# Performance work log

Hardware: AMD Instinct MI355X
Metric: run time of the kernel (lower is better)

## Reference

```python
import jax, jax.numpy as jnp
import numpy as np

N_NODES = 100000
N_EDGES = 1600000


def _degree_norms(src, dst, n):
    ones = jnp.ones(src.shape[0], dtype=jnp.float32)
    deg_out = jax.ops.segment_sum(ones, src, num_segments=n)
    deg_in = jax.ops.segment_sum(ones, dst, num_segments=n)
    src_norm = jax.lax.rsqrt(jnp.maximum(deg_out, 1.0))
    dst_norm = jax.lax.rsqrt(jnp.maximum(deg_in, 1.0))
    return src_norm, dst_norm


def _graph_conv(x, W, b, src, dst, src_norm, dst_norm, n):
    # DGL GraphConv, norm='both': D_dst^{-1/2} A D_src^{-1/2} X W + b
    # Apply W first (same math, smaller messages).
    h = x @ W                                  # [N, out]
    m = (h * src_norm[:, None])[src]           # [E, out] gather
    agg = jax.ops.segment_sum(m, dst, num_segments=n)  # [N, out] scatter-add
    return agg * dst_norm[:, None] + b


def setup_inputs() -> dict:
    key = jax.random.key(0)
    ks = jax.random.split(key, 10)
    inp = {
        "x": jax.random.normal(ks[0], (N_NODES, 128), dtype=jnp.float32),
        "src": jax.random.randint(ks[1], (N_EDGES,), 0, N_NODES, dtype=jnp.int32),
        "dst": jax.random.randint(ks[2], (N_EDGES,), 0, N_NODES, dtype=jnp.int32),
        "W1": jax.random.normal(ks[3], (128, 64), dtype=jnp.float32) * 0.08,
        "b1": jnp.zeros((64,), dtype=jnp.float32),
        "W2": jax.random.normal(ks[4], (64, 64), dtype=jnp.float32) * 0.12,
        "b2": jnp.zeros((64,), dtype=jnp.float32),
        "W3": jax.random.normal(ks[5], (64, 64), dtype=jnp.float32) * 0.12,
        "b3": jnp.zeros((64,), dtype=jnp.float32),
        "W4": jax.random.normal(ks[6], (64, 64), dtype=jnp.float32) * 0.12,
        "b4": jnp.zeros((64,), dtype=jnp.float32),
        "Wres": jax.random.normal(ks[7], (128, 64), dtype=jnp.float32) * 0.08,
        "bres": jnp.zeros((64,), dtype=jnp.float32),
        "Wop": jax.random.normal(ks[8], (64, 16), dtype=jnp.float32) * 0.12,
        "bop": jnp.zeros((16,), dtype=jnp.float32),
    }
    return inp


def reference(x, src, dst, W1, b1, W2, b2, W3, b3, W4, b4, Wres, bres, Wop, bop):
    n = x.shape[0]
    src_norm, dst_norm = _degree_norms(src, dst, n)
    res = x @ Wres + bres
    out = jax.nn.relu(_graph_conv(x, W1, b1, src, dst, src_norm, dst_norm, n))
    out = jax.nn.relu(_graph_conv(out, W2, b2, src, dst, src_norm, dst_norm, n))
    out = jax.nn.relu(_graph_conv(out, W3, b3, src, dst, src_norm, dst_norm, n))
    out = _graph_conv(out, W4, b4, src, dst, src_norm, dst_norm, n)
    out = jax.nn.relu(out + res)
    return out @ Wop + bop
```

## Files before the change

kernel.cpp:

```cpp
#include <hip/hip_runtime.h>
#include <cstdint>
#include <cstddef>


#define SLOTS 64
#define BCAP 5120
#define ACHUNK 4096

typedef __attribute__((ext_vector_type(8))) short bf16x8;
typedef __attribute__((ext_vector_type(4))) float f32x4;

__device__ __forceinline__ unsigned short f2bf(float f) {
  union { float f; unsigned u; } v; v.f = f;
  unsigned r = (v.u + 0x7fffu + ((v.u >> 16) & 1u)) >> 16;
  return (unsigned short)r;
}
__device__ __forceinline__ float bf2f(unsigned short h) {
  union { unsigned u; float f; } v; v.u = ((unsigned)h) << 16;
  return v.f;
}
__device__ __forceinline__ void bf2x2(unsigned u, float* lo, float* hi) {
  union { unsigned x; float f; } a, b;
  a.x = u << 16; b.x = u & 0xFFFF0000u;
  *lo = a.f; *hi = b.f;
}

__global__ void prep_kernel(const float* __restrict__ W1, const float* __restrict__ W2,
                            const float* __restrict__ W3, const float* __restrict__ W4,
                            const float* __restrict__ Wres,
                            unsigned short* __restrict__ WT,
                            int* __restrict__ gcur_d, int* __restrict__ gcur_s, int nbuck) {
  int i = blockIdx.x * blockDim.x + threadIdx.x;
  if (i < nbuck) { gcur_d[i] = 0; gcur_s[i] = 0; }
  if (i < 8192) {
    int c = i >> 7, k = i & 127;
    WT[i] = f2bf(W1[k * 64 + c]);
  } else if (i < 12288) {
    int j = i - 8192; int c = j >> 6, k = j & 63;
    WT[i] = f2bf(W2[k * 64 + c]);
  } else if (i < 16384) {
    int j = i - 12288; int c = j >> 6, k = j & 63;
    WT[i] = f2bf(W3[k * 64 + c]);
  } else if (i < 20480) {
    int j = i - 16384; int c = j >> 6, k = j & 63;
    WT[i] = f2bf(W4[k * 64 + c]);
  } else if (i < 28672) {
    int j = i - 20480; int c = j >> 7, k = j & 127;
    WT[i] = f2bf(Wres[k * 64 + c]);
  }
}

__global__ __launch_bounds__(256) void bucket_kernel(
    const int* __restrict__ src, const int* __restrict__ dst,
    int* __restrict__ gcur_d, int* __restrict__ gcur_s,
    unsigned* __restrict__ dbuck, unsigned char* __restrict__ sbuck,
    int E, int nbuck) {
  __shared__ int s_src[ACHUNK];
  __shared__ int s_dst[ACHUNK];
  __shared__ int run_d[512];
  __shared__ int run_s[512];
  const int t = threadIdx.x;
  const int base = blockIdx.x * ACHUNK;
  int cnt = E - base;
  if (cnt > ACHUNK) cnt = ACHUNK;

  for (int i = t; i < cnt; i += 256) {
    s_src[i] = src[base + i];
    s_dst[i] = dst[base + i];
  }
  for (int i = t; i < nbuck; i += 256) { run_d[i] = 0; run_s[i] = 0; }
  __syncthreads();
  for (int i = t; i < cnt; i += 256) {
    atomicAdd(&run_d[s_dst[i] >> 8], 1);
    atomicAdd(&run_s[s_src[i] >> 8], 1);
  }
  __syncthreads();
  {
    const int iters = (nbuck + 255) >> 8;
    for (int it = 0; it < iters; ++it) {
      int i = it * 256 + t;
      int hd = 0, hs = 0;
      if (i < nbuck) { hd = run_d[i]; hs = run_s[i]; }
      __syncthreads();
      if (i < nbuck) {
        run_d[i] = hd ? atomicAdd(&gcur_d[i], hd) : 0;
        run_s[i] = hs ? atomicAdd(&gcur_s[i], hs) : 0;
      }
      __syncthreads();
    }
  }
  for (int i = t; i < cnt; i += 256) {
    int d = s_dst[i], s = s_src[i];
    int bd = d >> 8;
    int pd = atomicAdd(&run_d[bd], 1);
    if (pd < BCAP) dbuck[(size_t)bd * BCAP + pd] = ((unsigned)(d & 255) << 24) | (unsigned)s;
    int bs = s >> 8;
    int ps = atomicAdd(&run_s[bs], 1);
    if (ps < BCAP) sbuck[(size_t)bs * BCAP + ps] = (unsigned char)(s & 255);
  }
}

__global__ __launch_bounds__(256) void csr_kernel(
    const unsigned* __restrict__ dbuck, const int* __restrict__ gcur_d,
    int* __restrict__ col, int* __restrict__ cnt_arr,
    float* __restrict__ dnorm, int N) {
  __shared__ int cur[256];
  const int b = blockIdx.x;
  const int t = threadIdx.x;
  const int node0 = b << 8;
  cur[t] = 0;
  __syncthreads();
  int cnt = gcur_d[b];
  if (cnt > BCAP) cnt = BCAP;
  const unsigned* p = dbuck + (size_t)b * BCAP;
  for (int i = t; i < cnt; i += 256) {
    unsigned e = p[i];
    int nl = e >> 24;
    int s = (int)(e & 0x00FFFFFFu);
    int pos = atomicAdd(&cur[nl], 1);
    if (pos < SLOTS) col[(size_t)(node0 + nl) * SLOTS + pos] = s;
  }
  __syncthreads();
  int node = node0 + t;
  if (node < N) {
    int c = cur[t];
    cnt_arr[node] = c;
    float d = (float)(c < 1 ? 1 : c);
    dnorm[node] = rsqrtf(d);
  }
}

__global__ __launch_bounds__(256) void degout_kernel(
    const unsigned char* __restrict__ sbuck, const int* __restrict__ gcur_s,
    float* __restrict__ snorm, int N) {
  __shared__ int cur[256];
  const int b = blockIdx.x;
  const int t = threadIdx.x;
  cur[t] = 0;
  __syncthreads();
  int cnt = gcur_s[b];
  if (cnt > BCAP) cnt = BCAP;
  const unsigned char* p = sbuck + (size_t)b * BCAP;
  for (int i = t; i < cnt; i += 256) atomicAdd(&cur[p[i]], 1);
  __syncthreads();
  int node = (b << 8) + t;
  if (node < N) {
    int c = cur[t];
    snorm[node] = rsqrtf((float)(c < 1 ? 1 : c));
  }
}

__global__ __launch_bounds__(256) void gemm_mfma_kernel(
    const unsigned short* __restrict__ X, const unsigned short* __restrict__ WT,
    const float* __restrict__ norm, unsigned short* __restrict__ out, int n) {
  __shared__ float ol[64][68];
  const int t = threadIdx.x;
  const int l = t & 63;
  const int w = t >> 6;
  const int node0 = blockIdx.x * 64;
  const int row = l & 15, kg = l >> 4;

  int arow = node0 + w * 16 + row;
  if (arow > n - 1) arow = n - 1;
  const unsigned short* ab = X + (size_t)arow * 64 + kg * 8;
  bf16x8 a0 = *(const bf16x8*)(ab);
  bf16x8 a1 = *(const bf16x8*)(ab + 32);

  f32x4 acc[4];
#pragma unroll
  for (int ct = 0; ct < 4; ct++) acc[ct] = (f32x4){0.f, 0.f, 0.f, 0.f};

#pragma unroll
  for (int ct = 0; ct < 4; ct++) {
    const unsigned short* wb = WT + (size_t)(ct * 16 + row) * 64 + kg * 8;
    bf16x8 b0 = *(const bf16x8*)(wb);
    bf16x8 b1 = *(const bf16x8*)(wb + 32);
    acc[ct] = __builtin_amdgcn_mfma_f32_16x16x32_bf16(a0, b0, acc[ct], 0, 0, 0);
    acc[ct] = __builtin_amdgcn_mfma_f32_16x16x32_bf16(a1, b1, acc[ct], 0, 0, 0);
  }

#pragma unroll
  for (int ct = 0; ct < 4; ct++)
#pragma unroll
    for (int i = 0; i < 4; i++)
      ol[w * 16 + kg * 4 + i][ct * 16 + row] = acc[ct][i];
  __syncthreads();

  {
    int r2 = t >> 2, cg = (t & 3) * 16;
    int node = node0 + r2;
    if (node < n) {
      float s = norm[node];
      unsigned short o[16];
#pragma unroll
      for (int i = 0; i < 16; i++) o[i] = f2bf(ol[r2][cg + i] * s);
      *(uint4*)&out[(size_t)node * 64 + cg] = *(const uint4*)&o[0];
      *(uint4*)&out[(size_t)node * 64 + cg + 8] = *(const uint4*)&o[8];
    }
  }
}

__global__ __launch_bounds__(256) void gemm1_mfma_kernel(
    const float* __restrict__ X, const unsigned short* __restrict__ W1T,
    const unsigned short* __restrict__ WresT, const float* __restrict__ bres,
    const float* __restrict__ norm,
    unsigned short* __restrict__ Hout, unsigned short* __restrict__ Rout, int n) {
  __shared__ unsigned short in_bf[64][136];
  __shared__ float ol[64][68];
  const int t = threadIdx.x;
  const int l = t & 63;
  const int w = t >> 6;
  const int node0 = blockIdx.x * 64;
  const int row = l & 15, kg = l >> 4;

  {
    int r = t >> 2, cb = (t & 3) * 32;
    int gi = node0 + r;
    unsigned short tmp[32];
    if (gi < n) {
      const float* s = X + (size_t)gi * 128 + cb;
#pragma unroll
      for (int q = 0; q < 32; q += 4) {
        float4 f = *(const float4*)(s + q);
        tmp[q] = f2bf(f.x); tmp[q + 1] = f2bf(f.y);
        tmp[q + 2] = f2bf(f.z); tmp[q + 3] = f2bf(f.w);
      }
    } else {
#pragma unroll
      for (int q = 0; q < 32; q++) tmp[q] = 0;
    }
#pragma unroll
    for (int q = 0; q < 32; q += 8)
      *(uint4*)&in_bf[r][cb + q] = *(const uint4*)&tmp[q];
  }
  __syncthreads();

  bf16x8 a[4];
#pragma unroll
  for (int kh = 0; kh < 4; kh++)
    a[kh] = *(const bf16x8*)&in_bf[w * 16 + row][kh * 32 + kg * 8];

  f32x4 acc[4], acc2[4];
#pragma unroll
  for (int ct = 0; ct < 4; ct++) {
    acc[ct] = (f32x4){0.f, 0.f, 0.f, 0.f};
    acc2[ct] = (f32x4){0.f, 0.f, 0.f, 0.f};
  }

#pragma unroll
  for (int kh = 0; kh < 4; kh++) {
#pragma unroll
    for (int ct = 0; ct < 4; ct++) {
      const unsigned short* wb1 = W1T + (size_t)(ct * 16 + row) * 128 + kh * 32 + kg * 8;
      const unsigned short* wbr = WresT + (size_t)(ct * 16 + row) * 128 + kh * 32 + kg * 8;
      bf16x8 b1 = *(const bf16x8*)(wb1);
      bf16x8 br = *(const bf16x8*)(wbr);
      acc[ct] = __builtin_amdgcn_mfma_f32_16x16x32_bf16(a[kh], b1, acc[ct], 0, 0, 0);
      acc2[ct] = __builtin_amdgcn_mfma_f32_16x16x32_bf16(a[kh], br, acc2[ct], 0, 0, 0);
    }
  }

#pragma unroll
  for (int ct = 0; ct < 4; ct++)
#pragma unroll
    for (int i = 0; i < 4; i++)
      ol[w * 16 + kg * 4 + i][ct * 16 + row] = acc[ct][i];
  __syncthreads();
  {
    int r2 = t >> 2, cg = (t & 3) * 16;
    int node = node0 + r2;
    if (node < n) {
      float s = norm[node];
      unsigned short o[16];
#pragma unroll
      for (int i = 0; i < 16; i++) o[i] = f2bf(ol[r2][cg + i] * s);
      *(uint4*)&Hout[(size_t)node * 64 + cg] = *(const uint4*)&o[0];
      *(uint4*)&Hout[(size_t)node * 64 + cg + 8] = *(const uint4*)&o[8];
    }
  }
  __syncthreads();

#pragma unroll
  for (int ct = 0; ct < 4; ct++)
#pragma unroll
    for (int i = 0; i < 4; i++)
      ol[w * 16 + kg * 4 + i][ct * 16 + row] = acc2[ct][i];
  __syncthreads();
  {
    int r2 = t >> 2, cg = (t & 3) * 16;
    int node = node0 + r2;
    if (node < n) {
      unsigned short o[16];
#pragma unroll
      for (int i = 0; i < 16; i++) o[i] = f2bf(ol[r2][cg + i] + bres[cg + i]);
      *(uint4*)&Rout[(size_t)node * 64 + cg] = *(const uint4*)&o[0];
      *(uint4*)&Rout[(size_t)node * 64 + cg + 8] = *(const uint4*)&o[8];
    }
  }
}

#define UNPACK_ADD(u, A)                         \
  { float f0, f1, f2, f3;                        \
    bf2x2((u).x, &f0, &f1);                      \
    bf2x2((u).y, &f2, &f3);                      \
    A[0] += f0; A[1] += f1; A[2] += f2; A[3] += f3; }

template <int RELU>
__global__ __launch_bounds__(256) void agg_kernel(
    const unsigned short* __restrict__ H, const int* __restrict__ cnt_arr,
    const int* __restrict__ col, const float* __restrict__ dnorm,
    const float* __restrict__ bias, unsigned short* __restrict__ O,
    int n) {
  const int lane = threadIdx.x & 63;
  const int g = lane >> 4;
  const int fl = lane & 15;
  const int wave = (blockIdx.x * blockDim.x + threadIdx.x) >> 6;
  const int nwaves = (gridDim.x * blockDim.x) >> 6;
  const uint2* __restrict__ H2 = (const uint2*)H;
  const float4 bb = ((const float4*)bias)[fl];

  for (int v0 = wave * 2; v0 < n; v0 += nwaves * 2) {
    const int v1 = v0 + 1;
    int cnt0 = cnt_arr[v0];
    int cnt1 = (v1 < n) ? cnt_arr[v1] : 0;
    if (cnt0 > SLOTS) cnt0 = SLOTS;
    if (cnt1 > SLOTS) cnt1 = SLOTS;
    const int* cp0 = col + (size_t)v0 * SLOTS;
    const int* cp1 = (v1 < n) ? col + (size_t)v1 * SLOTS : cp0;
    float a0[4] = {0.f, 0.f, 0.f, 0.f};
    float b0[4] = {0.f, 0.f, 0.f, 0.f};
    float a1[4] = {0.f, 0.f, 0.f, 0.f};
    float b1[4] = {0.f, 0.f, 0.f, 0.f};
    const int cmax = cnt0 > cnt1 ? cnt0 : cnt1;
    for (int j = 0; j < cmax; j += 16) {
      const int e0 = j + g;
      const int e1 = j + 4 + g;
      const int e2 = j + 8 + g;
      const int e3 = j + 12 + g;
      int c00 = cp0[e0], c01 = cp0[e1], c02 = cp0[e2], c03 = cp0[e3];
      int c10 = cp1[e0], c11 = cp1[e1], c12 = cp1[e2], c13 = cp1[e3];
      if (e0 < cnt0) { uint2 u = H2[(size_t)c00 * 16 + fl]; UNPACK_ADD(u, a0) }
      if (e1 < cnt0) { uint2 u = H2[(size_t)c01 * 16 + fl]; UNPACK_ADD(u, b0) }
      if (e2 < cnt0) { uint2 u = H2[(size_t)c02 * 16 + fl]; UNPACK_ADD(u, a0) }
      if (e3 < cnt0) { uint2 u = H2[(size_t)c03 * 16 + fl]; UNPACK_ADD(u, b0) }
      if (e0 < cnt1) { uint2 u = H2[(size_t)c10 * 16 + fl]; UNPACK_ADD(u, a1) }
      if (e1 < cnt1) { uint2 u = H2[(size_t)c11 * 16 + fl]; UNPACK_ADD(u, b1) }
      if (e2 < cnt1) { uint2 u = H2[(size_t)c12 * 16 + fl]; UNPACK_ADD(u, a1) }
      if (e3 < cnt1) { uint2 u = H2[(size_t)c13 * 16 + fl]; UNPACK_ADD(u, b1) }
    }
    float r0[4], r1[4];
#pragma unroll
    for (int i = 0; i < 4; i++) {
      float s0 = a0[i] + b0[i];
      s0 += __shfl_xor(s0, 16);
      s0 += __shfl_xor(s0, 32);
      r0[i] = s0;
      float s1 = a1[i] + b1[i];
      s1 += __shfl_xor(s1, 16);
      s1 += __shfl_xor(s1, 32);
      r1[i] = s1;
    }
    if (g == 0) {
      float d = dnorm[v0];
      float q0 = r0[0] * d + bb.x;
      float q1 = r0[1] * d + bb.y;
      float q2 = r0[2] * d + bb.z;
      float q3 = r0[3] * d + bb.w;
      if (RELU) {
        q0 = fmaxf(q0, 0.f); q1 = fmaxf(q1, 0.f);
        q2 = fmaxf(q2, 0.f); q3 = fmaxf(q3, 0.f);
      }
      ushort4 o;
      o.x = f2bf(q0); o.y = f2bf(q1); o.z = f2bf(q2); o.w = f2bf(q3);
      *(ushort4*)&O[(size_t)v0 * SLOTS + 4 * fl] = o;
    } else if (g == 1 && v1 < n) {
      float d = dnorm[v1];
      float q0 = r1[0] * d + bb.x;
      float q1 = r1[1] * d + bb.y;
      float q2 = r1[2] * d + bb.z;
      float q3 = r1[3] * d + bb.w;
      if (RELU) {
        q0 = fmaxf(q0, 0.f); q1 = fmaxf(q1, 0.f);
        q2 = fmaxf(q2, 0.f); q3 = fmaxf(q3, 0.f);
      }
      ushort4 o;
      o.x = f2bf(q0); o.y = f2bf(q1); o.z = f2bf(q2); o.w = f2bf(q3);
      *(ushort4*)&O[(size_t)v1 * SLOTS + 4 * fl] = o;
    }
  }
}

__global__ __launch_bounds__(256) void final_kernel(
    const unsigned short* __restrict__ O4, const unsigned short* __restrict__ R,
    const float* __restrict__ Wop, const float* __restrict__ bop,
    float* __restrict__ out, int n) {
  __shared__ float t_lds[64][68];
  __shared__ float wop_lds[64][16];
  const int t = threadIdx.x;
  const int node0 = blockIdx.x * 64;
  const int srow = t >> 2;
  const int scol = (t & 3) * 16;

  ((float4*)&wop_lds[0][0])[t] = ((const float4*)Wop)[t];

  {
    int gi = node0 + srow;
    float f[16];
    if (gi < n) {
      const unsigned short* po = O4 + (size_t)gi * 64 + scol;
      const unsigned short* pr = R + (size_t)gi * 64 + scol;
      uint4 uo0 = *(const uint4*)(po + 0);
      uint4 uo1 = *(const uint4*)(po + 8);
      uint4 ur0 = *(const uint4*)(pr + 0);
      uint4 ur1 = *(const uint4*)(pr + 8);
      float o0, o1, rr0, rr1;
#define ADDRELU2(UO, UR, idx)                         \
      bf2x2(UO, &o0, &o1); bf2x2(UR, &rr0, &rr1);     \
      f[idx] = fmaxf(o0 + rr0, 0.f);                  \
      f[idx + 1] = fmaxf(o1 + rr1, 0.f);
      ADDRELU2(uo0.x, ur0.x, 0)  ADDRELU2(uo0.y, ur0.y, 2)
      ADDRELU2(uo0.z, ur0.z, 4)  ADDRELU2(uo0.w, ur0.w, 6)
      ADDRELU2(uo1.x, ur1.x, 8)  ADDRELU2(uo1.y, ur1.y, 10)
      ADDRELU2(uo1.z, ur1.z, 12) ADDRELU2(uo1.w, ur1.w, 14)
#undef ADDRELU2
    } else {
#pragma unroll
      for (int j = 0; j < 16; j++) f[j] = 0.f;
    }
#pragma unroll
    for (int j = 0; j < 16; j += 4)
      *(float4*)&t_lds[srow][scol + j] = make_float4(f[j], f[j+1], f[j+2], f[j+3]);
  }
  __syncthreads();

  {
    int nn = t >> 2;
    int fg = t & 3;
    float4 a = ((const float4*)bop)[fg];
#pragma unroll 16
    for (int k = 0; k < 64; k++) {
      float tv = t_lds[nn][k];
      float4 w = *(const float4*)&wop_lds[k][fg * 4];
      a.x = fmaf(tv, w.x, a.x);
      a.y = fmaf(tv, w.y, a.y);
      a.z = fmaf(tv, w.z, a.z);
      a.w = fmaf(tv, w.w, a.w);
    }
    int node = node0 + nn;
    if (node < n) *(float4*)&out[(size_t)node * 16 + fg * 4] = a;
  }
}

extern "C" void kernel_launch(void* const* d_in, const int* in_sizes, int n_in,
                              void* d_out, int out_size, void* d_ws, size_t ws_size,
                              hipStream_t stream) {
  const float* x    = (const float*)d_in[0];
  const int*   src  = (const int*)d_in[1];
  const int*   dst  = (const int*)d_in[2];
  const float* W1   = (const float*)d_in[3];
  const float* b1   = (const float*)d_in[4];
  const float* W2   = (const float*)d_in[5];
  const float* b2   = (const float*)d_in[6];
  const float* W3   = (const float*)d_in[7];
  const float* b3   = (const float*)d_in[8];
  const float* W4   = (const float*)d_in[9];
  const float* b4   = (const float*)d_in[10];
  const float* Wres = (const float*)d_in[11];
  const float* bres = (const float*)d_in[12];
  const float* Wop  = (const float*)d_in[13];
  const float* bop  = (const float*)d_in[14];
  float* out = (float*)d_out;

  const int N = in_sizes[0] / 128;
  const int E = in_sizes[1];
  const int nbuck = (N + 255) >> 8;

  char* p = (char*)d_ws;
  auto alloc = [&](size_t b) {
    char* r = p;
    p += (b + 255) & ~(size_t)255;
    return r;
  };
  int*            gcur_d  = (int*)alloc((size_t)nbuck * 4);
  int*            gcur_s  = (int*)alloc((size_t)nbuck * 4);
  unsigned short* WT      = (unsigned short*)alloc(28672 * 2);
  unsigned*       dbuck   = (unsigned*)alloc((size_t)nbuck * BCAP * 4);
  unsigned char*  sbuck   = (unsigned char*)alloc((size_t)nbuck * BCAP);
  int*            col     = (int*)alloc((size_t)N * SLOTS * 4);
  int*            cnt_arr = (int*)alloc((size_t)N * 4);
  float*          snorm   = (float*)alloc((size_t)N * 4);
  float*          dnorm   = (float*)alloc((size_t)N * 4);
  unsigned short* Hbuf    = (unsigned short*)alloc((size_t)N * 64 * 2);
  unsigned short* Obuf    = (unsigned short*)alloc((size_t)N * 64 * 2);
  unsigned short* Rbuf    = (unsigned short*)alloc((size_t)N * 64 * 2);

  unsigned short* W1T   = WT;
  unsigned short* W2T   = WT + 8192;
  unsigned short* W3T   = WT + 12288;
  unsigned short* W4T   = WT + 16384;
  unsigned short* WresT = WT + 20480;

  prep_kernel<<<112, 256, 0, stream>>>(W1, W2, W3, W4, Wres, WT, gcur_d, gcur_s, nbuck);

  int ga = (E + ACHUNK - 1) / ACHUNK;
  bucket_kernel<<<ga, 256, 0, stream>>>(src, dst, gcur_d, gcur_s, dbuck, sbuck, E, nbuck);
  csr_kernel<<<nbuck, 256, 0, stream>>>(dbuck, gcur_d, col, cnt_arr, dnorm, N);
  degout_kernel<<<nbuck, 256, 0, stream>>>(sbuck, gcur_s, snorm, N);

  int gb = (N + 63) / 64;
  gemm1_mfma_kernel<<<gb, 256, 0, stream>>>(x, W1T, WresT, bres, snorm, Hbuf, Rbuf, N);
  agg_kernel<1><<<2048, 256, 0, stream>>>(Hbuf, cnt_arr, col, dnorm, b1, Obuf, N);
  gemm_mfma_kernel<<<gb, 256, 0, stream>>>(Obuf, W2T, snorm, Hbuf, N);
  agg_kernel<1><<<2048, 256, 0, stream>>>(Hbuf, cnt_arr, col, dnorm, b2, Obuf, N);
  gemm_mfma_kernel<<<gb, 256, 0, stream>>>(Obuf, W3T, snorm, Hbuf, N);
  agg_kernel<1><<<2048, 256, 0, stream>>>(Hbuf, cnt_arr, col, dnorm, b3, Obuf, N);
  gemm_mfma_kernel<<<gb, 256, 0, stream>>>(Obuf, W4T, snorm, Hbuf, N);
  agg_kernel<0><<<2048, 256, 0, stream>>>(Hbuf, cnt_arr, col, dnorm, b4, Obuf, N);
  final_kernel<<<gb, 256, 0, stream>>>(Obuf, Rbuf, Wop, bop, out, N);
}
```

Before: 326.7 us.

## Fuse aggregation with next-layer GEMM and final projection, shuffle-broadcast column indices

Each layer's neighbor aggregation now runs in a 512-thread block that covers 64 nodes. The block writes the ReLU'd bf16 result to LDS and immediately applies the next layer's weight with MFMA plus the source norm, so the intermediate Obuf round trip and the separate GEMM launches go away. The last aggregation is fused with the residual add, ReLU and output projection. Column indices are loaded once per wave and broadcast with shuffles instead of repeated global loads. The first GEMM converts fp32 input straight into registers rather than staging it through LDS. The cost is a fixed node-to-block mapping, which loses the grid-stride load balancing and uses less per-wave ILP (8 edges per iteration instead of 16).

```diff
diff --git a/kernel.cpp b/kernel.cpp
--- a/kernel.cpp
+++ b/kernel.cpp
@@ -15,15 +15,25 @@
   unsigned r = (v.u + 0x7fffu + ((v.u >> 16) & 1u)) >> 16;
   return (unsigned short)r;
 }
-__device__ __forceinline__ float bf2f(unsigned short h) {
-  union { unsigned u; float f; } v; v.u = ((unsigned)h) << 16;
-  return v.f;
-}
 __device__ __forceinline__ void bf2x2(unsigned u, float* lo, float* hi) {
   union { unsigned x; float f; } a, b;
   a.x = u << 16; b.x = u & 0xFFFF0000u;
   *lo = a.f; *hi = b.f;
 }
+__device__ __forceinline__ bf16x8 cvt8(float4 f0, float4 f1) {
+  bf16x8 v;
+  v[0] = (short)f2bf(f0.x); v[1] = (short)f2bf(f0.y);
+  v[2] = (short)f2bf(f0.z); v[3] = (short)f2bf(f0.w);
+  v[4] = (short)f2bf(f1.x); v[5] = (short)f2bf(f1.y);
+  v[6] = (short)f2bf(f1.z); v[7] = (short)f2bf(f1.w);
+  return v;
+}
+
+#define UNPACK_ADD(u, A)                         \
+  { float f0_, f1_, f2_, f3_;                    \
+    bf2x2((u).x, &f0_, &f1_);                    \
+    bf2x2((u).y, &f2_, &f3_);                    \
+    A[0] += f0_; A[1] += f1_; A[2] += f2_; A[3] += f3_; }
 
 __global__ void prep_kernel(const float* __restrict__ W1, const float* __restrict__ W2,
                             const float* __restrict__ W3, const float* __restrict__ W4,
@@ -150,9 +160,11 @@
   }
 }
 
-__global__ __launch_bounds__(256) void gemm_mfma_kernel(
-    const unsigned short* __restrict__ X, const unsigned short* __restrict__ WT,
-    const float* __restrict__ norm, unsigned short* __restrict__ out, int n) {
+__global__ __launch_bounds__(256) void gemm1_mfma_kernel(
+    const float* __restrict__ X, const unsigned short* __restrict__ W1T,
+    const unsigned short* __restrict__ WresT, const float* __restrict__ bres,
+    const float* __restrict__ norm,
+    unsigned short* __restrict__ Hout, unsigned short* __restrict__ Rout, int n) {
   __shared__ float ol[64][68];
   const int t = threadIdx.x;
   const int l = t & 63;
@@ -162,83 +174,14 @@
 
   int arow = node0 + w * 16 + row;
   if (arow > n - 1) arow = n - 1;
-  const unsigned short* ab = X + (size_t)arow * 64 + kg * 8;
-  bf16x8 a0 = *(const bf16x8*)(ab);
-  bf16x8 a1 = *(const bf16x8*)(ab + 32);
-
-  f32x4 acc[4];
-#pragma unroll
-  for (int ct = 0; ct < 4; ct++) acc[ct] = (f32x4){0.f, 0.f, 0.f, 0.f};
-
-#pragma unroll
-  for (int ct = 0; ct < 4; ct++) {
-    const unsigned short* wb = WT + (size_t)(ct * 16 + row) * 64 + kg * 8;
-    bf16x8 b0 = *(const bf16x8*)(wb);
-    bf16x8 b1 = *(const bf16x8*)(wb + 32);
-    acc[ct] = __builtin_amdgcn_mfma_f32_16x16x32_bf16(a0, b0, acc[ct], 0, 0, 0);
-    acc[ct] = __builtin_amdgcn_mfma_f32_16x16x32_bf16(a1, b1, acc[ct], 0, 0, 0);
-  }
-
-#pragma unroll
-  for (int ct = 0; ct < 4; ct++)
-#pragma unroll
-    for (int i = 0; i < 4; i++)
-      ol[w * 16 + kg * 4 + i][ct * 16 + row] = acc[ct][i];
-  __syncthreads();
-
-  {
-    int r2 = t >> 2, cg = (t & 3) * 16;
-    int node = node0 + r2;
-    if (node < n) {
-      float s = norm[node];
-      unsigned short o[16];
-#pragma unroll
-      for (int i = 0; i < 16; i++) o[i] = f2bf(ol[r2][cg + i] * s);
-      *(uint4*)&out[(size_t)node * 64 + cg] = *(const uint4*)&o[0];
-      *(uint4*)&out[(size_t)node * 64 + cg + 8] = *(const uint4*)&o[8];
-    }
-  }
-}
-
-__global__ __launch_bounds__(256) void gemm1_mfma_kernel(
-    const float* __restrict__ X, const unsigned short* __restrict__ W1T,
-    const unsigned short* __restrict__ WresT, const float* __restrict__ bres,
-    const float* __restrict__ norm,
-    unsigned short* __restrict__ Hout, unsigned short* __restrict__ Rout, int n) {
-  __shared__ unsigned short in_bf[64][136];
-  __shared__ float ol[64][68];
-  const int t = threadIdx.x;
-  const int l = t & 63;
-  const int w = t >> 6;
-  const int node0 = blockIdx.x * 64;
-  const int row = l & 15, kg = l >> 4;
-
-  {
-    int r = t >> 2, cb = (t & 3) * 32;
-    int gi = node0 + r;
-    unsigned short tmp[32];
-    if (gi < n) {
-      const float* s = X + (size_t)gi * 128 + cb;
-#pragma unroll
-      for (int q = 0; q < 32; q += 4) {
-        float4 f = *(const float4*)(s + q);
-        tmp[q] = f2bf(f.x); tmp[q + 1] = f2bf(f.y);
-        tmp[q + 2] = f2bf(f.z); tmp[q + 3] = f2bf(f.w);
-      }
-    } else {
-#pragma unroll
-      for (int q = 0; q < 32; q++) tmp[q] = 0;
-    }
-#pragma unroll
-    for (int q = 0; q < 32; q += 8)
-      *(uint4*)&in_bf[r][cb + q] = *(const uint4*)&tmp[q];
-  }
-  __syncthreads();
-
+  const float* ap = X + (size_t)arow * 128 + kg * 8;
   bf16x8 a[4];
 #pragma unroll
-  for (int kh = 0; kh < 4; kh++)
-    a[kh] = *(const bf16x8*)&in_bf[w * 16 + row][kh * 32 + kg * 8];
+  for (int kh = 0; kh < 4; kh++) {
+    float4 f0 = *(const float4*)(ap + kh * 32);
+    float4 f1 = *(const float4*)(ap + kh * 32 + 4);
+    a[kh] = cvt8(f0, f1);
+  }
 
   f32x4 acc[4], acc2[4];
 #pragma unroll
@@ -279,7 +222,6 @@
     }
   }
   __syncthreads();
-
 #pragma unroll
   for (int ct = 0; ct < 4; ct++)
 #pragma unroll
@@ -299,54 +241,46 @@
   }
 }
 
-#define UNPACK_ADD(u, A)                         \
-  { float f0, f1, f2, f3;                        \
-    bf2x2((u).x, &f0, &f1);                      \
-    bf2x2((u).y, &f2, &f3);                      \
-    A[0] += f0; A[1] += f1; A[2] += f2; A[3] += f3; }
-
-template <int RELU>
-__global__ __launch_bounds__(256) void agg_kernel(
+__global__ __launch_bounds__(512) void agg_gemm_kernel(
     const unsigned short* __restrict__ H, const int* __restrict__ cnt_arr,
     const int* __restrict__ col, const float* __restrict__ dnorm,
-    const float* __restrict__ bias, unsigned short* __restrict__ O,
-    int n) {
-  const int lane = threadIdx.x & 63;
-  const int g = lane >> 4;
+    const float* __restrict__ bias, const unsigned short* __restrict__ WTn,
+    const float* __restrict__ snorm, unsigned short* __restrict__ Hn, int N) {
+  __shared__ unsigned short ot[64][72];
+  const int t = threadIdx.x;
+  const int w = t >> 6;
+  const int lane = t & 63;
+  const int sub = lane >> 4;
   const int fl = lane & 15;
-  const int wave = (blockIdx.x * blockDim.x + threadIdx.x) >> 6;
-  const int nwaves = (gridDim.x * blockDim.x) >> 6;
+  const int node0 = blockIdx.x * 64;
   const uint2* __restrict__ H2 = (const uint2*)H;
   const float4 bb = ((const float4*)bias)[fl];
 
-  for (int v0 = wave * 2; v0 < n; v0 += nwaves * 2) {
-    const int v1 = v0 + 1;
-    int cnt0 = cnt_arr[v0];
-    int cnt1 = (v1 < n) ? cnt_arr[v1] : 0;
+  for (int p = 0; p < 4; p++) {
+    const int r0i = w * 8 + p * 2;
+    const int v0 = node0 + r0i, v1 = v0 + 1;
+    int cnt0 = (v0 < N) ? cnt_arr[v0] : 0;
+    int cnt1 = (v1 < N) ? cnt_arr[v1] : 0;
     if (cnt0 > SLOTS) cnt0 = SLOTS;
     if (cnt1 > SLOTS) cnt1 = SLOTS;
-    const int* cp0 = col + (size_t)v0 * SLOTS;
-    const int* cp1 = (v1 < n) ? col + (size_t)v1 * SLOTS : cp0;
+    int cv0 = (lane < cnt0) ? col[(size_t)v0 * SLOTS + lane] : 0;
+    int cv1 = (lane < cnt1) ? col[(size_t)v1 * SLOTS + lane] : 0;
     float a0[4] = {0.f, 0.f, 0.f, 0.f};
     float b0[4] = {0.f, 0.f, 0.f, 0.f};
     float a1[4] = {0.f, 0.f, 0.f, 0.f};
     float b1[4] = {0.f, 0.f, 0.f, 0.f};
     const int cmax = cnt0 > cnt1 ? cnt0 : cnt1;
-    for (int j = 0; j < cmax; j += 16) {
-      const int e0 = j + g;
-      const int e1 = j + 4 + g;
-      const int e2 = j + 8 + g;
-      const int e3 = j + 12 + g;
-      int c00 = cp0[e0], c01 = cp0[e1], c02 = cp0[e2], c03 = cp0[e3];
-      int c10 = cp1[e0], c11 = cp1[e1], c12 = cp1[e2], c13 = cp1[e3];
+    for (int j = 0; j < cmax; j += 8) {
+      const int e0 = j + sub;
+      const int e1 = j + 4 + sub;
+      int c00 = __shfl(cv0, e0);
+      int c01 = __shfl(cv0, e1);
+      int c10 = __shfl(cv1, e0);
+      int c11 = __shfl(cv1, e1);
       if (e0 < cnt0) { uint2 u = H2[(size_t)c00 * 16 + fl]; UNPACK_ADD(u, a0) }
+      if (e0 < cnt1) { uint2 u = H2[(size_t)c10 * 16 + fl]; UNPACK_ADD(u, a1) }
       if (e1 < cnt0) { uint2 u = H2[(size_t)c01 * 16 + fl]; UNPACK_ADD(u, b0) }
-      if (e2 < cnt0) { uint2 u = H2[(size_t)c02 * 16 + fl]; UNPACK_ADD(u, a0) }
-      if (e3 < cnt0) { uint2 u = H2[(size_t)c03 * 16 + fl]; UNPACK_ADD(u, b0) }
-      if (e0 < cnt1) { uint2 u = H2[(size_t)c10 * 16 + fl]; UNPACK_ADD(u, a1) }
       if (e1 < cnt1) { uint2 u = H2[(size_t)c11 * 16 + fl]; UNPACK_ADD(u, b1) }
-      if (e2 < cnt1) { uint2 u = H2[(size_t)c12 * 16 + fl]; UNPACK_ADD(u, a1) }
-      if (e3 < cnt1) { uint2 u = H2[(size_t)c13 * 16 + fl]; UNPACK_ADD(u, b1) }
     }
     float r0[4], r1[4];
 #pragma unroll
@@ -360,94 +294,190 @@
       s1 += __shfl_xor(s1, 32);
       r1[i] = s1;
     }
-    if (g == 0) {
-      float d = dnorm[v0];
-      float q0 = r0[0] * d + bb.x;
-      float q1 = r0[1] * d + bb.y;
-      float q2 = r0[2] * d + bb.z;
-      float q3 = r0[3] * d + bb.w;
-      if (RELU) {
-        q0 = fmaxf(q0, 0.f); q1 = fmaxf(q1, 0.f);
-        q2 = fmaxf(q2, 0.f); q3 = fmaxf(q3, 0.f);
+    if (sub == 0) {
+      ushort4 o = {0, 0, 0, 0};
+      if (v0 < N) {
+        float d = dnorm[v0];
+        o.x = f2bf(fmaxf(r0[0] * d + bb.x, 0.f));
+        o.y = f2bf(fmaxf(r0[1] * d + bb.y, 0.f));
+        o.z = f2bf(fmaxf(r0[2] * d + bb.z, 0.f));
+        o.w = f2bf(fmaxf(r0[3] * d + bb.w, 0.f));
       }
-      ushort4 o;
-      o.x = f2bf(q0); o.y = f2bf(q1); o.z = f2bf(q2); o.w = f2bf(q3);
-      *(ushort4*)&O[(size_t)v0 * SLOTS + 4 * fl] = o;
-    } else if (g == 1 && v1 < n) {
-      float d = dnorm[v1];
-      float q0 = r1[0] * d + bb.x;
-      float q1 = r1[1] * d + bb.y;
-      float q2 = r1[2] * d + bb.z;
-      float q3 = r1[3] * d + bb.w;
-      if (RELU) {
-        q0 = fmaxf(q0, 0.f); q1 = fmaxf(q1, 0.f);
-        q2 = fmaxf(q2, 0.f); q3 = fmaxf(q3, 0.f);
+      *(ushort4*)&ot[r0i][4 * fl] = o;
+    } else if (sub == 1) {
+      ushort4 o = {0, 0, 0, 0};
+      if (v1 < N) {
+        float d = dnorm[v1];
+        o.x = f2bf(fmaxf(r1[0] * d + bb.x, 0.f));
+        o.y = f2bf(fmaxf(r1[1] * d + bb.y, 0.f));
+        o.z = f2bf(fmaxf(r1[2] * d + bb.z, 0.f));
+        o.w = f2bf(fmaxf(r1[3] * d + bb.w, 0.f));
       }
-      ushort4 o;
-      o.x = f2bf(q0); o.y = f2bf(q1); o.z = f2bf(q2); o.w = f2bf(q3);
-      *(ushort4*)&O[(size_t)v1 * SLOTS + 4 * fl] = o;
-    }
-  }
-}
-
-__global__ __launch_bounds__(256) void final_kernel(
-    const unsigned short* __restrict__ O4, const unsigned short* __restrict__ R,
+      *(ushort4*)&ot[r0i + 1][4 * fl] = o;
+    }
+  }
+  __syncthreads();
+
+  const int g4 = w & 3, cp = w >> 2;
+  const int row = lane & 15, kg = lane >> 4;
+  bf16x8 A0 = *(const bf16x8*)&ot[g4 * 16 + row][kg * 8];
+  bf16x8 A1 = *(const bf16x8*)&ot[g4 * 16 + row][32 + kg * 8];
+  __syncthreads();
+
+  f32x4 acc[2];
+  acc[0] = (f32x4){0.f, 0.f, 0.f, 0.f};
+  acc[1] = (f32x4){0.f, 0.f, 0.f, 0.f};
+#pragma unroll
+  for (int cc = 0; cc < 2; cc++) {
+    const int ct = cp * 2 + cc;
+    const unsigned short* wb = WTn + (size_t)(ct * 16 + row) * 64 + kg * 8;
+    bf16x8 B0 = *(const bf16x8*)(wb);
+    bf16x8 B1 = *(const bf16x8*)(wb + 32);
+    acc[cc] = __builtin_amdgcn_mfma_f32_16x16x32_bf16(A0, B0, acc[cc], 0, 0, 0);
+    acc[cc] = __builtin_amdgcn_mfma_f32_16x16x32_bf16(A1, B1, acc[cc], 0, 0, 0);
+  }
+
+  float sn[4];
+#pragma unroll
+  for (int i = 0; i < 4; i++) {
+    int node = node0 + g4 * 16 + kg * 4 + i;
+    sn[i] = (node < N) ? snorm[node] : 0.f;
+  }
+#pragma unroll
+  for (int cc = 0; cc < 2; cc++) {
+    const int ct = cp * 2 + cc;
+#pragma unroll
+    for (int i = 0; i < 4; i++)
+      ot[g4 * 16 + kg * 4 + i][ct * 16 + row] = f2bf(acc[cc][i] * sn[i]);
+  }
+  __syncthreads();
+
+  {
+    int r2 = t >> 3, cb = (t & 7) * 8;
+    int node = node0 + r2;
+    if (node < N)
+      *(uint4*)&Hn[(size_t)node * 64 + cb] = *(const uint4*)&ot[r2][cb];
+  }
+}
+
+__global__ __launch_bounds__(512) void agg_final_kernel(
+    const unsigned short* __restrict__ H, const int* __restrict__ cnt_arr,
+    const int* __restrict__ col, const float* __restrict__ dnorm,
+    const float* __restrict__ bias, const unsigned short* __restrict__ R,
     const float* __restrict__ Wop, const float* __restrict__ bop,
-    float* __restrict__ out, int n) {
-  __shared__ float t_lds[64][68];
+    float* __restrict__ out, int N) {
+  __shared__ float tl[64][68];
   __shared__ float wop_lds[64][16];
   const int t = threadIdx.x;
+  const int w = t >> 6;
+  const int lane = t & 63;
+  const int sub = lane >> 4;
+  const int fl = lane & 15;
   const int node0 = blockIdx.x * 64;
-  const int srow = t >> 2;
-  const int scol = (t & 3) * 16;
-
-  ((float4*)&wop_lds[0][0])[t] = ((const float4*)Wop)[t];
+  const uint2* __restrict__ H2 = (const uint2*)H;
+  const float4 bb = ((const float4*)bias)[fl];
+
+  if (t < 256) ((float4*)&wop_lds[0][0])[t] = ((const float4*)Wop)[t];
+
+  for (int p = 0; p < 4; p++) {
+    const int r0i = w * 8 + p * 2;
+    const int v0 = node0 + r0i, v1 = v0 + 1;
+    int cnt0 = (v0 < N) ? cnt_arr[v0] : 0;
+    int cnt1 = (v1 < N) ? cnt_arr[v1] : 0;
+    if (cnt0 > SLOTS) cnt0 = SLOTS;
+    if (cnt1 > SLOTS) cnt1 = SLOTS;
+    int cv0 = (lane < cnt0) ? col[(size_t)v0 * SLOTS + lane] : 0;
+    int cv1 = (lane < cnt1) ? col[(size_t)v1 * SLOTS + lane] : 0;
+    float a0[4] = {0.f, 0.f, 0.f, 0.f};
+    float b0[4] = {0.f, 0.f, 0.f, 0.f};
+    float a1[4] = {0.f, 0.f, 0.f, 0.f};
+    float b1[4] = {0.f, 0.f, 0.f, 0.f};
+    const int cmax = cnt0 > cnt1 ? cnt0 : cnt1;
+    for (int j = 0; j < cmax; j += 8) {
+      const int e0 = j + sub;
+      const int e1 = j + 4 + sub;
+      int c00 = __shfl(cv0, e0);
+      int c01 = __shfl(cv0, e1);
+      int c10 = __shfl(cv1, e0);
+      int c11 = __shfl(cv1, e1);
+      if (e0 < cnt0) { uint2 u = H2[(size_t)c00 * 16 + fl]; UNPACK_ADD(u, a0) }
+      if (e0 < cnt1) { uint2 u = H2[(size_t)c10 * 16 + fl]; UNPACK_ADD(u, a1) }
+      if (e1 < cnt0) { uint2 u = H2[(size_t)c01 * 16 + fl]; UNPACK_ADD(u, b0) }
+      if (e1 < cnt1) { uint2 u = H2[(size_t)c11 * 16 + fl]; UNPACK_ADD(u, b1) }
+    }
+    float r0[4], r1[4];
+#pragma unroll
+    for (int i = 0; i < 4; i++) {
+      float s0 = a0[i] + b0[i];
+      s0 += __shfl_xor(s0, 16);
+      s0 += __shfl_xor(s0, 32);
+      r0[i] = s0;
+      float s1 = a1[i] + b1[i];
+      s1 += __shfl_xor(s1, 16);
+      s1 += __shfl_xor(s1, 32);
+      r1[i] = s1;
+    }
+    if (sub == 0) {
+      float4 o = make_float4(0.f, 0.f, 0.f, 0.f);
+      if (v0 < N) {
+        float d = dnorm[v0];
+        o.x = r0[0] * d + bb.x;
+        o.y = r0[1] * d + bb.y;
+        o.z = r0[2] * d + bb.z;
+        o.w = r0[3] * d + bb.w;
+      }
+      *(float4*)&tl[r0i][4 * fl] = o;
+    } else if (sub == 1) {
+      float4 o = make_float4(0.f, 0.f, 0.f, 0.f);
+      if (v1 < N) {
+        float d = dnorm[v1];
+        o.x = r1[0] * d + bb.x;
+        o.y = r1[1] * d + bb.y;
+        o.z = r1[2] * d + bb.z;
+        o.w = r1[3] * d + bb.w;
+      }
+      *(float4*)&tl[r0i + 1][4 * fl] = o;
+    }
+  }
+  __syncthreads();
 
   {
-    int gi = node0 + srow;
-    float f[16];
-    if (gi < n) {
-      const unsigned short* po = O4 + (size_t)gi * 64 + scol;
-      const unsigned short* pr = R + (size_t)gi * 64 + scol;
-      uint4 uo0 = *(const uint4*)(po + 0);
-      uint4 uo1 = *(const uint4*)(po + 8);
-      uint4 ur0 = *(const uint4*)(pr + 0);
-      uint4 ur1 = *(const uint4*)(pr + 8);
-      float o0, o1, rr0, rr1;
-#define ADDRELU2(UO, UR, idx)                         \
-      bf2x2(UO, &o0, &o1); bf2x2(UR, &rr0, &rr1);     \
-      f[idx] = fmaxf(o0 + rr0, 0.f);                  \
-      f[idx + 1] = fmaxf(o1 + rr1, 0.f);
-      ADDRELU2(uo0.x, ur0.x, 0)  ADDRELU2(uo0.y, ur0.y, 2)
-      ADDRELU2(uo0.z, ur0.z, 4)  ADDRELU2(uo0.w, ur0.w, 6)
-      ADDRELU2(uo1.x, ur1.x, 8)  ADDRELU2(uo1.y, ur1.y, 10)
-      ADDRELU2(uo1.z, ur1.z, 12) ADDRELU2(uo1.w, ur1.w, 14)
-#undef ADDRELU2
-    } else {
-#pragma unroll
-      for (int j = 0; j < 16; j++) f[j] = 0.f;
-    }
-#pragma unroll
-    for (int j = 0; j < 16; j += 4)
-      *(float4*)&t_lds[srow][scol + j] = make_float4(f[j], f[j+1], f[j+2], f[j+3]);
-  }
-  __syncthreads();
-
-  {
+    int r2 = t >> 3, cb = (t & 7) * 8;
+    int node = node0 + r2;
+    if (node < N) {
+      uint4 ur = *(const uint4*)&R[(size_t)node * 64 + cb];
+      float f0, f1;
+      bf2x2(ur.x, &f0, &f1);
+      tl[r2][cb + 0] = fmaxf(tl[r2][cb + 0] + f0, 0.f);
+      tl[r2][cb + 1] = fmaxf(tl[r2][cb + 1] + f1, 0.f);
+      bf2x2(ur.y, &f0, &f1);
+      tl[r2][cb + 2] = fmaxf(tl[r2][cb + 2] + f0, 0.f);
+      tl[r2][cb + 3] = fmaxf(tl[r2][cb + 3] + f1, 0.f);
+      bf2x2(ur.z, &f0, &f1);
+      tl[r2][cb + 4] = fmaxf(tl[r2][cb + 4] + f0, 0.f);
+      tl[r2][cb + 5] = fmaxf(tl[r2][cb + 5] + f1, 0.f);
+      bf2x2(ur.w, &f0, &f1);
+      tl[r2][cb + 6] = fmaxf(tl[r2][cb + 6] + f0, 0.f);
+      tl[r2][cb + 7] = fmaxf(tl[r2][cb + 7] + f1, 0.f);
+    }
+  }
+  __syncthreads();
+
+  if (t < 256) {
     int nn = t >> 2;
     int fg = t & 3;
     float4 a = ((const float4*)bop)[fg];
 #pragma unroll 16
     for (int k = 0; k < 64; k++) {
-      float tv = t_lds[nn][k];
-      float4 w = *(const float4*)&wop_lds[k][fg * 4];
-      a.x = fmaf(tv, w.x, a.x);
-      a.y = fmaf(tv, w.y, a.y);
-      a.z = fmaf(tv, w.z, a.z);
-      a.w = fmaf(tv, w.w, a.w);
+      float tv = tl[nn][k];
+      float4 wv = *(const float4*)&wop_lds[k][fg * 4];
+      a.x = fmaf(tv, wv.x, a.x);
+      a.y = fmaf(tv, wv.y, a.y);
+      a.z = fmaf(tv, wv.z, a.z);
+      a.w = fmaf(tv, wv.w, a.w);
     }
     int node = node0 + nn;
-    if (node < n) *(float4*)&out[(size_t)node * 16 + fg * 4] = a;
+    if (node < N) *(float4*)&out[(size_t)node * 16 + fg * 4] = a;
   }
 }
 
@@ -490,8 +520,8 @@
   int*            cnt_arr = (int*)alloc((size_t)N * 4);
   float*          snorm   = (float*)alloc((size_t)N * 4);
   float*          dnorm   = (float*)alloc((size_t)N * 4);
-  unsigned short* Hbuf    = (unsigned short*)alloc((size_t)N * 64 * 2);
-  unsigned short* Obuf    = (unsigned short*)alloc((size_t)N * 64 * 2);
+  unsigned short* Ha      = (unsigned short*)alloc((size_t)N * 64 * 2);
+  unsigned short* Hb      = (unsigned short*)alloc((size_t)N * 64 * 2);
   unsigned short* Rbuf    = (unsigned short*)alloc((size_t)N * 64 * 2);
 
   unsigned short* W1T   = WT;
@@ -508,13 +538,9 @@
   degout_kernel<<<nbuck, 256, 0, stream>>>(sbuck, gcur_s, snorm, N);
 
   int gb = (N + 63) / 64;
-  gemm1_mfma_kernel<<<gb, 256, 0, stream>>>(x, W1T, WresT, bres, snorm, Hbuf, Rbuf, N);
-  agg_kernel<1><<<2048, 256, 0, stream>>>(Hbuf, cnt_arr, col, dnorm, b1, Obuf, N);
-  gemm_mfma_kernel<<<gb, 256, 0, stream>>>(Obuf, W2T, snorm, Hbuf, N);
-  agg_kernel<1><<<2048, 256, 0, stream>>>(Hbuf, cnt_arr, col, dnorm, b2, Obuf, N);
-  gemm_mfma_kernel<<<gb, 256, 0, stream>>>(Obuf, W3T, snorm, Hbuf, N);
-  agg_kernel<1><<<2048, 256, 0, stream>>>(Hbuf, cnt_arr, col, dnorm, b3, Obuf, N);
-  gemm_mfma_kernel<<<gb, 256, 0, stream>>>(Obuf, W4T, snorm, Hbuf, N);
-  agg_kernel<0><<<2048, 256, 0, stream>>>(Hbuf, cnt_arr, col, dnorm, b4, Obuf, N);
-  final_kernel<<<gb, 256, 0, stream>>>(Obuf, Rbuf, Wop, bop, out, N);
-}
+  gemm1_mfma_kernel<<<gb, 256, 0, stream>>>(x, W1T, WresT, bres, snorm, Ha, Rbuf, N);
+  agg_gemm_kernel<<<gb, 512, 0, stream>>>(Ha, cnt_arr, col, dnorm, b1, W2T, snorm, Hb, N);
+  agg_gemm_kernel<<<gb, 512, 0, stream>>>(Hb, cnt_arr, col, dnorm, b2, W3T, snorm, Ha, N);
+  agg_gemm_kernel<<<gb, 512, 0, stream>>>(Ha, cnt_arr, col, dnorm, b3, W4T, snorm, Hb, N);
+  agg_final_kernel<<<gb, 512, 0, stream>>>(Hb, cnt_arr, col, dnorm, b4, Rbuf, Wop, bop, out, N);
+}
```

Result: faster. 316.0 us (-3.3%).
